# Performance work log

Measured on AMD Instinct MI355X. Metric: run time of the kernel, lower is better.

## Reference

```python
import jax, jax.numpy as jnp
import numpy as np

N_HEAD = 16

def _ln(x, g, b):
    m = jnp.mean(x, axis=-1, keepdims=True)
    v = jnp.var(x, axis=-1, keepdims=True)
    return (x - m) / jnp.sqrt(v + 1e-5) * g + b

def setup_inputs() -> dict:
    key = jax.random.key(0)
    B, T, D, L, V = 2, 1024, 1024, 4, 32000
    ks = jax.random.split(key, 8)
    s = 0.02
    return {
        'input_ids': jax.random.randint(ks[0], (B, T), 0, V),
        'wte': jax.random.normal(ks[1], (V, D), jnp.float32) * s,
        'wpe': jax.random.normal(ks[2], (T, D), jnp.float32) * s,
        'ln1_g': jnp.ones((L, D), jnp.float32), 'ln1_b': jnp.zeros((L, D), jnp.float32),
        'w_qkv': jax.random.normal(ks[3], (L, D, 3 * D), jnp.float32) * s,
        'b_qkv': jnp.zeros((L, 3 * D), jnp.float32),
        'w_proj': jax.random.normal(ks[4], (L, D, D), jnp.float32) * s,
        'b_proj': jnp.zeros((L, D), jnp.float32),
        'ln2_g': jnp.ones((L, D), jnp.float32), 'ln2_b': jnp.zeros((L, D), jnp.float32),
        'w_fc1': jax.random.normal(ks[5], (L, D, 4 * D), jnp.float32) * s,
        'b_fc1': jnp.zeros((L, 4 * D), jnp.float32),
        'w_fc2': jax.random.normal(ks[6], (L, 4 * D, D), jnp.float32) * s,
        'b_fc2': jnp.zeros((L, D), jnp.float32),
        'lnf_g': jnp.ones((D,), jnp.float32), 'lnf_b': jnp.zeros((D,), jnp.float32),
        'w_lm': jax.random.normal(ks[7], (D, V), jnp.float32) * s,
    }

def reference(input_ids, wte, wpe, ln1_g, ln1_b, w_qkv, b_qkv, w_proj, b_proj,
              ln2_g, ln2_b, w_fc1, b_fc1, w_fc2, b_fc2, lnf_g, lnf_b, w_lm):
    B, T = input_ids.shape
    D = wte.shape[1]
    H = N_HEAD
    hd = D // H
    mask = jnp.tril(jnp.ones((T, T), dtype=bool))  # causal
    x = wte[input_ids] + wpe[:T][None, :, :]  # token + position embeddings

    def layer(h, p):
        g1, bb1, Wq, bq, Wp, bp, g2, bb2, W1, b1, W2, b2 = p
        a = _ln(h, g1, bb1)
        qkv = a @ Wq + bq
        q, k, v = jnp.split(qkv, 3, axis=-1)
        q = q.reshape(B, T, H, hd)
        k = k.reshape(B, T, H, hd)
        v = v.reshape(B, T, H, hd)
        att = jnp.einsum('bqhd,bkhd->bhqk', q, k) / jnp.sqrt(jnp.float32(hd))
        att = jnp.where(mask[None, None], att, -jnp.inf)
        att = jax.nn.softmax(att, axis=-1)
        y = jnp.einsum('bhqk,bkhd->bqhd', att, v).reshape(B, T, D)
        h = h + y @ Wp + bp
        m = _ln(h, g2, bb2)
        # torch nn.GELU default is exact erf variant
        m = jax.nn.gelu(m @ W1 + b1, approximate=False) @ W2 + b2
        h = h + m
        return h, None

    params = (ln1_g, ln1_b, w_qkv, b_qkv, w_proj, b_proj,
              ln2_g, ln2_b, w_fc1, b_fc1, w_fc2, b_fc2)
    h, _ = jax.lax.scan(layer, x, params)
    h = _ln(h, lnf_g, lnf_b)
    logits = h @ w_lm  # [B, T, vocab]
    return logits
```

## Files before the change

### kernel.cpp

```cpp
#include <hip/hip_runtime.h>
#include <hip/hip_bf16.h>
#include <math.h>

typedef __attribute__((ext_vector_type(4))) float f32x4;
typedef __attribute__((ext_vector_type(8))) short short8;
typedef __attribute__((ext_vector_type(4))) unsigned short ushort4v;

__device__ __forceinline__ unsigned short f2bf(float f) {
    return __builtin_bit_cast(unsigned short, __float2bfloat16(f));
}

__device__ __forceinline__ void gload16(const void* g, void* l) {
    __builtin_amdgcn_global_load_lds(
        (const __attribute__((address_space(1))) unsigned int*)g,
        (__attribute__((address_space(3))) unsigned int*)l, 16, 0, 0);
}

__global__ __launch_bounds__(256)
void tc_kernel(const float* __restrict__ in, __hip_bfloat16* __restrict__ out,
               int N, int K)
{
    __shared__ float tile[64][65];
    const size_t loff = (size_t)blockIdx.z * K * N;
    const int k0 = blockIdx.x * 64, n0 = blockIdx.y * 64;
    const int t = threadIdx.x;
    {
        int kk = t >> 2, nb = (t & 3) * 16;
        const float* src = in + loff + (size_t)(k0 + kk) * N + n0 + nb;
        #pragma unroll
        for (int j = 0; j < 4; ++j) {
            float4 v = *(const float4*)(src + j * 4);
            tile[kk][nb + j*4 + 0] = v.x; tile[kk][nb + j*4 + 1] = v.y;
            tile[kk][nb + j*4 + 2] = v.z; tile[kk][nb + j*4 + 3] = v.w;
        }
    }
    __syncthreads();
    {
        int nn = t >> 2, kb = (t & 3) * 16;
        __hip_bfloat16* dst = out + loff + (size_t)(n0 + nn) * K + k0 + kb;
        short8 w0, w1;
        #pragma unroll
        for (int j = 0; j < 8; ++j) w0[j] = (short)f2bf(tile[kb + j][nn]);
        #pragma unroll
        for (int j = 0; j < 8; ++j) w1[j] = (short)f2bf(tile[kb + 8 + j][nn]);
        *(short8*)dst = w0;
        *(short8*)(dst + 8) = w1;
    }
}

__global__ __launch_bounds__(256)
void embed_kernel(const int* __restrict__ ids, const float* __restrict__ wte,
                  const float* __restrict__ wpe, float* __restrict__ h)
{
    int row  = blockIdx.x;
    int tpos = row & 1023;
    int id   = ids[row];
    float4 a = ((const float4*)(wte + (size_t)id * 1024))[threadIdx.x];
    float4 p = ((const float4*)(wpe + (size_t)tpos * 1024))[threadIdx.x];
    float4 o; o.x = a.x + p.x; o.y = a.y + p.y; o.z = a.z + p.z; o.w = a.w + p.w;
    ((float4*)(h + (size_t)row * 1024))[threadIdx.x] = o;
}

__global__ __launch_bounds__(256)
void ln_kernel(const float* __restrict__ x, const float* __restrict__ g,
               const float* __restrict__ b, __hip_bfloat16* __restrict__ out)
{
    size_t row = blockIdx.x;
    float4 v = ((const float4*)(x + row * 1024))[threadIdx.x];
    float s  = v.x + v.y + v.z + v.w;
    float s2 = v.x*v.x + v.y*v.y + v.z*v.z + v.w*v.w;
    #pragma unroll
    for (int off = 32; off; off >>= 1) {
        s  += __shfl_xor(s, off);
        s2 += __shfl_xor(s2, off);
    }
    __shared__ float rs[4], rs2[4];
    int wave = threadIdx.x >> 6;
    if ((threadIdx.x & 63) == 0) { rs[wave] = s; rs2[wave] = s2; }
    __syncthreads();
    s  = rs[0] + rs[1] + rs[2] + rs[3];
    s2 = rs2[0] + rs2[1] + rs2[2] + rs2[3];
    float mean = s * (1.f / 1024.f);
    float var  = s2 * (1.f / 1024.f) - mean * mean;
    float rstd = rsqrtf(var + 1e-5f);
    float4 gg = ((const float4*)g)[threadIdx.x];
    float4 bb = ((const float4*)b)[threadIdx.x];
    ushort4v ov;
    ov[0] = f2bf((v.x - mean) * rstd * gg.x + bb.x);
    ov[1] = f2bf((v.y - mean) * rstd * gg.y + bb.y);
    ov[2] = f2bf((v.z - mean) * rstd * gg.z + bb.z);
    ov[3] = f2bf((v.w - mean) * rstd * gg.w + bb.w);
    ((ushort4v*)(out + row * 1024))[threadIdx.x] = ov;
}

template<bool OUT_BF16, bool GELU_ACT, bool NT, int BN, bool SWZ>
__global__ __launch_bounds__(256)
void gemm_bf16(const __hip_bfloat16* __restrict__ A,
               const __hip_bfloat16* __restrict__ Bt,
               const float* __restrict__ bias, const float* __restrict__ resid,
               void* __restrict__ Cout, int M, int N, int K, int GN)
{
    __shared__ unsigned char smem[32768 + 2 * BN * 128];
    int mblk, pnl;
    if (SWZ) {
        int bid = blockIdx.x;
        int x = bid & 7, j = bid >> 3;
        int pw = GN >> 3;
        int whole = pw * 128;
        if (bid < whole) { pnl = x + 8 * (j >> 4); mblk = j & 15; }
        else { int r = bid - whole; pnl = (pw << 3) + (r >> 4); mblk = r & 15; }
    } else {
        mblk = blockIdx.x; pnl = blockIdx.y;
    }
    const int m0 = mblk * 128;
    const int n0 = pnl * BN;
    const int t    = threadIdx.x;
    const int lane = t & 63;
    const int wave = t >> 6;
    constexpr int NF = (BN == 128) ? 4 : 2;
    const int wm = (BN == 128) ? (wave >> 1) * 64 : (wave & 1) * 64;
    const int wn = (BN == 128) ? (wave & 1) * 64 : (wave >> 1) * 32;

    f32x4 acc[4][NF];
    #pragma unroll
    for (int i = 0; i < 4; ++i)
        #pragma unroll
        for (int j = 0; j < NF; ++j) {
            acc[i][j][0] = 0.f; acc[i][j][1] = 0.f; acc[i][j][2] = 0.f; acc[i][j][3] = 0.f;
        }

    const int l8 = lane >> 3;
    const int lc = (lane & 7) ^ l8;
    constexpr int NB = NF;
    const __hip_bfloat16* agp[4];
    const __hip_bfloat16* bgp[NB];
    int aoff[4];
    int boff[NB];
    #pragma unroll
    for (int i = 0; i < 4; ++i) {
        int row = wave * 32 + i * 8 + l8;
        agp[i]  = A + (size_t)(m0 + row) * K + lc * 8;
        aoff[i] = (wave * 32 + i * 8) * 128;
    }
    #pragma unroll
    for (int i = 0; i < NB; ++i) {
        int row = wave * (BN / 4) + i * 8 + l8;
        bgp[i]  = Bt + (size_t)(n0 + row) * K + lc * 8;
        boff[i] = (wave * (BN / 4) + i * 8) * 128;
    }
    const int aBufOff[2] = { 0, 16384 };
    const int bBufOff[2] = { 32768, 32768 + BN * 128 };

    #pragma unroll
    for (int i = 0; i < 4; ++i)  gload16(agp[i], smem + aBufOff[0] + aoff[i]);
    #pragma unroll
    for (int i = 0; i < NB; ++i) gload16(bgp[i], smem + bBufOff[0] + boff[i]);
    __syncthreads();

    int cur = 0;
    for (int k0 = 0; k0 < K; k0 += 64) {
        if (k0 + 64 < K) {
            #pragma unroll
            for (int i = 0; i < 4; ++i)
                gload16(agp[i] + k0 + 64, smem + aBufOff[cur ^ 1] + aoff[i]);
            #pragma unroll
            for (int i = 0; i < NB; ++i)
                gload16(bgp[i] + k0 + 64, smem + bBufOff[cur ^ 1] + boff[i]);
        }
        const unsigned char* abuf = smem + aBufOff[cur];
        const unsigned char* bbuf = smem + bBufOff[cur];
        const int lr = lane & 15;
        const int lk = lane >> 4;
        #pragma unroll
        for (int ks = 0; ks < 2; ++ks) {
            int chunk = ks * 4 + lk;
            short8 af[4], bfr[NF];
            #pragma unroll
            for (int m = 0; m < 4; ++m) {
                int row = wm + m * 16 + lr;
                af[m] = *(const short8*)(abuf + row * 128 + ((chunk * 16) ^ ((row & 7) << 4)));
            }
            #pragma unroll
            for (int n = 0; n < NF; ++n) {
                int nn = wn + n * 16 + lr;
                bfr[n] = *(const short8*)(bbuf + nn * 128 + ((chunk * 16) ^ ((nn & 7) << 4)));
            }
            #pragma unroll
            for (int m = 0; m < 4; ++m)
                #pragma unroll
                for (int n = 0; n < NF; ++n)
                    acc[m][n] = __builtin_amdgcn_mfma_f32_16x16x32_bf16(af[m], bfr[n], acc[m][n], 0, 0, 0);
        }
        __syncthreads();
        cur ^= 1;
    }

    const int lr = lane & 15;
    const int lq = lane >> 4;
    float bv[NF];
    #pragma unroll
    for (int n = 0; n < NF; ++n)
        bv[n] = bias ? bias[n0 + wn + n * 16 + lr] : 0.f;
    #pragma unroll
    for (int m = 0; m < 4; ++m) {
        int rbase = m0 + wm + m * 16 + lq * 4;
        #pragma unroll
        for (int j = 0; j < 4; ++j) {
            int row = rbase + j;
            #pragma unroll
            for (int n = 0; n < NF; ++n) {
                int col = n0 + wn + n * 16 + lr;
                float v = acc[m][n][j] + bv[n];
                if (resid) v += resid[(size_t)row * N + col];
                if (GELU_ACT) v = 0.5f * v * (1.f + erff(v * 0.70710678118654752f));
                if (OUT_BF16) {
                    ((__hip_bfloat16*)Cout)[(size_t)row * N + col] = __float2bfloat16(v);
                } else if (NT) {
                    __builtin_nontemporal_store(v, (float*)Cout + (size_t)row * N + col);
                } else {
                    ((float*)Cout)[(size_t)row * N + col] = v;
                }
            }
        }
    }
}

__global__ __launch_bounds__(256)
void attn_mfma(const __hip_bfloat16* __restrict__ qkv,
               __hip_bfloat16* __restrict__ y)
{
    __shared__ short Qs[64][72];
    __shared__ short Ps[64][72];
    __shared__ unsigned char Kl[8192];
    __shared__ short Vt[64][72];

    const int bid = blockIdx.x;
    const int p   = bid >> 5;
    const int qt  = (p < 8) ? (15 - 2 * p) : (2 * (p - 8));
    const int bh  = bid & 31;
    const int b = bh >> 4, h = bh & 15;
    const int t = threadIdx.x, lane = t & 63, w = t >> 6;
    const int lr = lane & 15, lg = lane >> 4;
    const size_t base = (size_t)b * 1024 * 3072;
    const int qbase = qt * 64;

    {
        int row = t >> 2, c = t & 3;
        const short8* qsrc = (const short8*)(qkv + base + (size_t)(qbase + row) * 3072 + h * 64);
        *(short8*)&Qs[row][c * 8]      = qsrc[c];
        *(short8*)&Qs[row][c * 8 + 32] = qsrc[c + 4];
    }
    __syncthreads();

    short8 aq0 = *(const short8*)&Qs[w * 16 + lr][0 * 32 + lg * 8];
    short8 aq1 = *(const short8*)&Qs[w * 16 + lr][1 * 32 + lg * 8];

    f32x4 oacc[4];
    #pragma unroll
    for (int dt = 0; dt < 4; ++dt) { oacc[dt][0]=0.f; oacc[dt][1]=0.f; oacc[dt][2]=0.f; oacc[dt][3]=0.f; }
    float lsum[4] = {0.f, 0.f, 0.f, 0.f};

    const int ntiles = qt + 1;
    const int kkey = t >> 2, kc = t & 3;
    const int vkey = t & 63, vc = t >> 6;

    for (int tile = 0; tile < ntiles; ++tile) {
        const int kb = tile * 64;
        {
            const short8* ksrc = (const short8*)(qkv + base + (size_t)(kb + kkey) * 3072 + 1024 + h * 64);
            short8 k0 = ksrc[kc], k1 = ksrc[kc + 4];
            int rb = kkey * 128, sw = (kkey & 7) << 4;
            *(short8*)(Kl + rb + ((kc * 16) ^ sw)) = k0;
            *(short8*)(Kl + rb + (((kc + 4) * 16) ^ sw)) = k1;

            const short8* vsrc = (const short8*)(qkv + base + (size_t)(kb + vkey) * 3072 + 2048 + h * 64);
            short8 v0 = vsrc[vc], v1 = vsrc[vc + 4];
            #pragma unroll
            for (int j = 0; j < 8; ++j) Vt[vc * 8 + j][vkey] = v0[j];
            #pragma unroll
            for (int j = 0; j < 8; ++j) Vt[(vc + 4) * 8 + j][vkey] = v1[j];
        }
        __syncthreads();

        f32x4 sacc[4];
        #pragma unroll
        for (int kt = 0; kt < 4; ++kt) { sacc[kt][0]=0.f; sacc[kt][1]=0.f; sacc[kt][2]=0.f; sacc[kt][3]=0.f; }
        #pragma unroll
        for (int ks = 0; ks < 2; ++ks) {
            short8 aq = ks ? aq1 : aq0;
            #pragma unroll
            for (int kt = 0; kt < 4; ++kt) {
                int krow = kt * 16 + lr;
                short8 bk = *(const short8*)(Kl + krow * 128 + (((ks * 4 + lg) * 16) ^ ((krow & 7) << 4)));
                sacc[kt] = __builtin_amdgcn_mfma_f32_16x16x32_bf16(aq, bk, sacc[kt], 0, 0, 0);
            }
        }

        #pragma unroll
        for (int kt = 0; kt < 4; ++kt) {
            int key = kb + kt * 16 + lr;
            #pragma unroll
            for (int j = 0; j < 4; ++j) {
                int q = qbase + w * 16 + lg * 4 + j;
                float pv = (key <= q) ? __expf(sacc[kt][j] * 0.125f) : 0.f;
                lsum[j] += pv;
                Ps[w * 16 + lg * 4 + j][kt * 16 + lr] = (short)f2bf(pv);
            }
        }

        #pragma unroll
        for (int ks = 0; ks < 2; ++ks) {
            short8 ap = *(const short8*)&Ps[w * 16 + lr][ks * 32 + lg * 8];
            #pragma unroll
            for (int dt = 0; dt < 4; ++dt) {
                short8 bv = *(const short8*)&Vt[dt * 16 + lr][ks * 32 + lg * 8];
                oacc[dt] = __builtin_amdgcn_mfma_f32_16x16x32_bf16(ap, bv, oacc[dt], 0, 0, 0);
            }
        }
        __syncthreads();
    }

    #pragma unroll
    for (int j = 0; j < 4; ++j) {
        float l = lsum[j];
        l += __shfl_xor(l, 1); l += __shfl_xor(l, 2);
        l += __shfl_xor(l, 4); l += __shfl_xor(l, 8);
        float inv = 1.f / l;
        int qrow = qbase + w * 16 + lg * 4 + j;
        __hip_bfloat16* dst = y + (size_t)(b * 1024 + qrow) * 1024 + h * 64;
        #pragma unroll
        for (int dt = 0; dt < 4; ++dt)
            dst[dt * 16 + lr] = __float2bfloat16(oacc[dt][j] * inv);
    }
}

extern "C" void kernel_launch(void* const* d_in, const int* in_sizes, int n_in,
                              void* d_out, int out_size, void* d_ws, size_t ws_size,
                              hipStream_t stream)
{
    (void)in_sizes; (void)n_in; (void)out_size; (void)ws_size;

    const int*   ids    = (const int*)d_in[0];
    const float* wte    = (const float*)d_in[1];
    const float* wpe    = (const float*)d_in[2];
    const float* ln1_g  = (const float*)d_in[3];
    const float* ln1_b  = (const float*)d_in[4];
    const float* w_qkv  = (const float*)d_in[5];
    const float* b_qkv  = (const float*)d_in[6];
    const float* w_proj = (const float*)d_in[7];
    const float* b_proj = (const float*)d_in[8];
    const float* ln2_g  = (const float*)d_in[9];
    const float* ln2_b  = (const float*)d_in[10];
    const float* w_fc1  = (const float*)d_in[11];
    const float* b_fc1  = (const float*)d_in[12];
    const float* w_fc2  = (const float*)d_in[13];
    const float* b_fc2  = (const float*)d_in[14];
    const float* lnf_g  = (const float*)d_in[15];
    const float* lnf_b  = (const float*)d_in[16];
    const float* w_lm   = (const float*)d_in[17];

    char* ws = (char*)d_ws;
    __hip_bfloat16* abuf_bf = (__hip_bfloat16*)ws;
    float*          hbuf    = (float*)(ws + (4u<<20));
    __hip_bfloat16* qkvb_bf = (__hip_bfloat16*)(ws + (12u<<20));
    __hip_bfloat16* ybuf_bf = (__hip_bfloat16*)(ws + (24u<<20));
    __hip_bfloat16* mbuf_bf = (__hip_bfloat16*)(ws + (28u<<20));
    __hip_bfloat16* wlm_bf  = (__hip_bfloat16*)(ws + (4u<<20));

    __hip_bfloat16* wq_bf = (__hip_bfloat16*)d_out;
    __hip_bfloat16* wp_bf = wq_bf + (size_t)4*1024*3072;
    __hip_bfloat16* w1_bf = wp_bf + (size_t)4*1024*1024;
    __hip_bfloat16* w2_bf = w1_bf + (size_t)4*1024*4096;

    float* out = (float*)d_out;

    tc_kernel<<<dim3(16, 48, 4), 256, 0, stream>>>(w_qkv,  wq_bf, 3072, 1024);
    tc_kernel<<<dim3(16, 16, 4), 256, 0, stream>>>(w_proj, wp_bf, 1024, 1024);
    tc_kernel<<<dim3(16, 64, 4), 256, 0, stream>>>(w_fc1,  w1_bf, 4096, 1024);
    tc_kernel<<<dim3(64, 16, 4), 256, 0, stream>>>(w_fc2,  w2_bf, 1024, 4096);

    embed_kernel<<<2048, 256, 0, stream>>>(ids, wte, wpe, hbuf);

    for (int l = 0; l < 4; ++l) {
        ln_kernel<<<2048, 256, 0, stream>>>(hbuf, ln1_g + l*1024, ln1_b + l*1024, abuf_bf);
        gemm_bf16<true,false,false,128,false><<<dim3(16, 24), 256, 0, stream>>>(
            abuf_bf, wq_bf + (size_t)l*1024*3072, b_qkv + l*3072, nullptr, qkvb_bf, 2048, 3072, 1024, 24);
        attn_mfma<<<512, 256, 0, stream>>>(qkvb_bf, ybuf_bf);
        gemm_bf16<false,false,false,64,false><<<dim3(16, 16), 256, 0, stream>>>(
            ybuf_bf, wp_bf + (size_t)l*1024*1024, b_proj + l*1024, hbuf, hbuf, 2048, 1024, 1024, 16);
        ln_kernel<<<2048, 256, 0, stream>>>(hbuf, ln2_g + l*1024, ln2_b + l*1024, abuf_bf);
        gemm_bf16<true,true,false,128,false><<<dim3(16, 32), 256, 0, stream>>>(
            abuf_bf, w1_bf + (size_t)l*1024*4096, b_fc1 + l*4096, nullptr, mbuf_bf, 2048, 4096, 1024, 32);
        gemm_bf16<false,false,false,64,false><<<dim3(16, 16), 256, 0, stream>>>(
            mbuf_bf, w2_bf + (size_t)l*4096*1024, b_fc2 + l*1024, hbuf, hbuf, 2048, 1024, 4096, 16);
    }

    ln_kernel<<<2048, 256, 0, stream>>>(hbuf, lnf_g, lnf_b, abuf_bf);
    tc_kernel<<<dim3(16, 500, 1), 256, 0, stream>>>(w_lm, wlm_bf, 32000, 1024);
    gemm_bf16<false,false,true,128,true><<<16*250, 256, 0, stream>>>(
        abuf_bf, wlm_bf, nullptr, nullptr, out, 2048, 32000, 1024, 250);
}
```

Measured before the change: 915.2 us.

## Prefetch next K/V tile into registers in attention; swizzle all GEMM block orders

The attention kernel now loads the next K/V tile from global memory into registers while computing on the current tile, then writes it to LDS after a barrier. This hides global load latency behind the MFMA work at the cost of extra registers. Separately, every GEMM launch now uses the grouped block-index swizzle with a 1D grid, which was previously used only for the LM head, to improve L2 reuse of weight panels.

```diff
diff --git a/kernel.cpp b/kernel.cpp
--- a/kernel.cpp
+++ b/kernel.cpp
@@ -93,7 +93,7 @@
     ((ushort4v*)(out + row * 1024))[threadIdx.x] = ov;
 }
 
-template<bool OUT_BF16, bool GELU_ACT, bool NT, int BN, bool SWZ>
+template<bool OUT_BF16, bool GELU_ACT, bool NT, int BN>
 __global__ __launch_bounds__(256)
 void gemm_bf16(const __hip_bfloat16* __restrict__ A,
                const __hip_bfloat16* __restrict__ Bt,
@@ -102,15 +102,13 @@
 {
     __shared__ unsigned char smem[32768 + 2 * BN * 128];
     int mblk, pnl;
-    if (SWZ) {
+    {
         int bid = blockIdx.x;
         int x = bid & 7, j = bid >> 3;
         int pw = GN >> 3;
         int whole = pw * 128;
         if (bid < whole) { pnl = x + 8 * (j >> 4); mblk = j & 15; }
         else { int r = bid - whole; pnl = (pw << 3) + (r >> 4); mblk = r & 15; }
-    } else {
-        mblk = blockIdx.x; pnl = blockIdx.y;
     }
     const int m0 = mblk * 128;
     const int n0 = pnl * BN;
@@ -264,24 +262,34 @@
     const int kkey = t >> 2, kc = t & 3;
     const int vkey = t & 63, vc = t >> 6;
 
+    short8 rk0, rk1, rv0, rv1;
+    {
+        const short8* ksrc = (const short8*)(qkv + base + (size_t)kkey * 3072 + 1024 + h * 64);
+        rk0 = ksrc[kc]; rk1 = ksrc[kc + 4];
+        const short8* vsrc = (const short8*)(qkv + base + (size_t)vkey * 3072 + 2048 + h * 64);
+        rv0 = vsrc[vc]; rv1 = vsrc[vc + 4];
+    }
+    {
+        int rb = kkey * 128, sw = (kkey & 7) << 4;
+        *(short8*)(Kl + rb + ((kc * 16) ^ sw)) = rk0;
+        *(short8*)(Kl + rb + (((kc + 4) * 16) ^ sw)) = rk1;
+        #pragma unroll
+        for (int j = 0; j < 8; ++j) Vt[vc * 8 + j][vkey] = rv0[j];
+        #pragma unroll
+        for (int j = 0; j < 8; ++j) Vt[(vc + 4) * 8 + j][vkey] = rv1[j];
+    }
+    __syncthreads();
+
     for (int tile = 0; tile < ntiles; ++tile) {
+        if (tile + 1 < ntiles) {
+            const int kb2 = (tile + 1) * 64;
+            const short8* ksrc = (const short8*)(qkv + base + (size_t)(kb2 + kkey) * 3072 + 1024 + h * 64);
+            rk0 = ksrc[kc]; rk1 = ksrc[kc + 4];
+            const short8* vsrc = (const short8*)(qkv + base + (size_t)(kb2 + vkey) * 3072 + 2048 + h * 64);
+            rv0 = vsrc[vc]; rv1 = vsrc[vc + 4];
+        }
+
         const int kb = tile * 64;
-        {
-            const short8* ksrc = (const short8*)(qkv + base + (size_t)(kb + kkey) * 3072 + 1024 + h * 64);
-            short8 k0 = ksrc[kc], k1 = ksrc[kc + 4];
-            int rb = kkey * 128, sw = (kkey & 7) << 4;
-            *(short8*)(Kl + rb + ((kc * 16) ^ sw)) = k0;
-            *(short8*)(Kl + rb + (((kc + 4) * 16) ^ sw)) = k1;
-
-            const short8* vsrc = (const short8*)(qkv + base + (size_t)(kb + vkey) * 3072 + 2048 + h * 64);
-            short8 v0 = vsrc[vc], v1 = vsrc[vc + 4];
-            #pragma unroll
-            for (int j = 0; j < 8; ++j) Vt[vc * 8 + j][vkey] = v0[j];
-            #pragma unroll
-            for (int j = 0; j < 8; ++j) Vt[(vc + 4) * 8 + j][vkey] = v1[j];
-        }
-        __syncthreads();
-
         f32x4 sacc[4];
         #pragma unroll
         for (int kt = 0; kt < 4; ++kt) { sacc[kt][0]=0.f; sacc[kt][1]=0.f; sacc[kt][2]=0.f; sacc[kt][3]=0.f; }
@@ -317,7 +325,18 @@
                 oacc[dt] = __builtin_amdgcn_mfma_f32_16x16x32_bf16(ap, bv, oacc[dt], 0, 0, 0);
             }
         }
-        __syncthreads();
+
+        if (tile + 1 < ntiles) {
+            __syncthreads();
+            int rb = kkey * 128, sw = (kkey & 7) << 4;
+            *(short8*)(Kl + rb + ((kc * 16) ^ sw)) = rk0;
+            *(short8*)(Kl + rb + (((kc + 4) * 16) ^ sw)) = rk1;
+            #pragma unroll
+            for (int j = 0; j < 8; ++j) Vt[vc * 8 + j][vkey] = rv0[j];
+            #pragma unroll
+            for (int j = 0; j < 8; ++j) Vt[(vc + 4) * 8 + j][vkey] = rv1[j];
+            __syncthreads();
+        }
     }
 
     #pragma unroll
@@ -383,20 +402,20 @@
 
     for (int l = 0; l < 4; ++l) {
         ln_kernel<<<2048, 256, 0, stream>>>(hbuf, ln1_g + l*1024, ln1_b + l*1024, abuf_bf);
-        gemm_bf16<true,false,false,128,false><<<dim3(16, 24), 256, 0, stream>>>(
+        gemm_bf16<true,false,false,128><<<16*24, 256, 0, stream>>>(
             abuf_bf, wq_bf + (size_t)l*1024*3072, b_qkv + l*3072, nullptr, qkvb_bf, 2048, 3072, 1024, 24);
         attn_mfma<<<512, 256, 0, stream>>>(qkvb_bf, ybuf_bf);
-        gemm_bf16<false,false,false,64,false><<<dim3(16, 16), 256, 0, stream>>>(
+        gemm_bf16<false,false,false,64><<<16*16, 256, 0, stream>>>(
             ybuf_bf, wp_bf + (size_t)l*1024*1024, b_proj + l*1024, hbuf, hbuf, 2048, 1024, 1024, 16);
         ln_kernel<<<2048, 256, 0, stream>>>(hbuf, ln2_g + l*1024, ln2_b + l*1024, abuf_bf);
-        gemm_bf16<true,true,false,128,false><<<dim3(16, 32), 256, 0, stream>>>(
+        gemm_bf16<true,true,false,128><<<16*32, 256, 0, stream>>>(
             abuf_bf, w1_bf + (size_t)l*1024*4096, b_fc1 + l*4096, nullptr, mbuf_bf, 2048, 4096, 1024, 32);
-        gemm_bf16<false,false,false,64,false><<<dim3(16, 16), 256, 0, stream>>>(
+        gemm_bf16<false,false,false,64><<<16*16, 256, 0, stream>>>(
             mbuf_bf, w2_bf + (size_t)l*4096*1024, b_fc2 + l*1024, hbuf, hbuf, 2048, 1024, 4096, 16);
     }
 
     ln_kernel<<<2048, 256, 0, stream>>>(hbuf, lnf_g, lnf_b, abuf_bf);
     tc_kernel<<<dim3(16, 500, 1), 256, 0, stream>>>(w_lm, wlm_bf, 32000, 1024);
-    gemm_bf16<false,false,true,128,true><<<16*250, 256, 0, stream>>>(
+    gemm_bf16<false,false,true,128><<<16*250, 256, 0, stream>>>(
         abuf_bf, wlm_bf, nullptr, nullptr, out, 2048, 32000, 1024, 250);
 }
```

Result: faster. 893.8 us (-2.3%).
